# Optimization experiments

Hardware: AMD Instinct MI355X
Metric: run time of the kernel (lower is better)

## Reference

```python
import jax, jax.numpy as jnp
import numpy as np

NF = 64      # num_feat
NFR = 5      # num_frames
G = 8        # offset/deformable groups
CENTER = NFR // 2
K = 9        # 3x3 taps


def conv3x3(x, w, b):
    y = jax.lax.conv_general_dilated(x, w, (1, 1), 'SAME',
                                     dimension_numbers=('NCHW', 'OIHW', 'NCHW'))
    return y + b[None, :, None, None]


def mdcn(x, offsets, masks, w, b):
    # x: [B,C,H,W]; offsets: [B,2*G*K,H,W] (layout g,k,(y,x)); masks: [B,G*K,H,W]
    B, C, H, W = x.shape
    Cg = C // G
    off = offsets.reshape(B, G, K, 2, H, W)
    oy, ox = off[:, :, :, 0], off[:, :, :, 1]          # [B,G,K,H,W]
    m = masks.reshape(B, G, K, H, W)
    ky = jnp.repeat(jnp.arange(3), 3) - 1              # [K]
    kx = jnp.tile(jnp.arange(3), 3) - 1
    base_y = (ky[:, None, None] + jnp.arange(H)[None, :, None]).astype(x.dtype)  # [K,H,1]
    base_x = (kx[:, None, None] + jnp.arange(W)[None, None, :]).astype(x.dtype)  # [K,1,W]
    py = oy + base_y[None, None]                        # [B,G,K,H,W]
    px = ox + base_x[None, None]
    y0f = jnp.floor(py); x0f = jnp.floor(px)
    ty = py - y0f; tx = px - x0f
    y0 = y0f.astype(jnp.int32); x0 = x0f.astype(jnp.int32)
    xg = x.reshape(B, G, Cg, H * W)

    def gather(yi, xi):
        valid = (yi >= 0) & (yi < H) & (xi >= 0) & (xi < W)
        yc = jnp.clip(yi, 0, H - 1); xc = jnp.clip(xi, 0, W - 1)
        idx = (yc * W + xc).reshape(B, G, 1, K * H * W)
        idx = jnp.broadcast_to(idx, (B, G, Cg, K * H * W))
        v = jnp.take_along_axis(xg, idx, axis=3).reshape(B, G, Cg, K, H, W)
        return v * valid.reshape(B, G, 1, K, H, W)

    v00 = gather(y0, x0); v01 = gather(y0, x0 + 1)
    v10 = gather(y0 + 1, x0); v11 = gather(y0 + 1, x0 + 1)
    ty_ = ty[:, :, None]; tx_ = tx[:, :, None]          # [B,G,1,K,H,W]
    samp = (v00 * (1 - ty_) * (1 - tx_) + v01 * (1 - ty_) * tx_ +
            v10 * ty_ * (1 - tx_) + v11 * ty_ * tx_)
    samp = samp * m[:, :, None]                          # modulation
    wr = w.reshape(-1, G, Cg, K)                         # [Cout,G,Cg,K]
    out = jnp.einsum('bgckhw,ogck->bohw', samp, wr)
    return out + b[None, :, None, None]


def setup_inputs():
    key = jax.random.key(0)
    ks = jax.random.split(key, 16)
    def mk(k, shape, fan_in):
        return jax.random.normal(k, shape, jnp.float32) * (1.0 / np.sqrt(fan_in))
    B, H, W = 1, 160, 160
    return {
        'x':   jax.random.normal(ks[0], (B, NFR, 4, H, W), jnp.float32),
        'fw1': mk(ks[1], (NF, 4, 3, 3), 4 * 9),   'fb1': jnp.zeros((NF,), jnp.float32),
        'fw2': mk(ks[2], (NF, NF, 3, 3), NF * 9), 'fb2': jnp.zeros((NF,), jnp.float32),
        'fw3': mk(ks[3], (NF, NF, 3, 3), NF * 9), 'fb3': jnp.zeros((NF,), jnp.float32),
        'ow1': mk(ks[4], (NF, 2 * NF, 3, 3), 2 * NF * 9), 'ob1': jnp.zeros((NF,), jnp.float32),
        'ow2': mk(ks[5], (NF, NF, 3, 3), NF * 9),         'ob2': jnp.zeros((NF,), jnp.float32),
        'ow3': mk(ks[6], (G * 27, NF, 3, 3), NF * 9) * 0.1,
        'ob3': jnp.zeros((G * 27,), jnp.float32),
        'dw':  mk(ks[7], (NF, NF, 3, 3), NF * 9), 'db': jnp.zeros((NF,), jnp.float32),
    }


def reference(x, fw1, fb1, fw2, fb2, fw3, fb3, ow1, ob1, ow2, ob2, ow3, ob3, dw, db):
    B, N, C, H, W = x.shape
    f = x.reshape(B * N, C, H, W)
    f = jax.nn.relu(conv3x3(f, fw1, fb1))
    f = jax.nn.relu(conv3x3(f, fw2, fb2))
    f = jax.nn.relu(conv3x3(f, fw3, fb3))
    feats = f.reshape(B, N, NF, H, W)
    ref = feats[:, CENTER]                               # [B,NF,H,W]
    nc = np.array([i for i in range(N) if i != CENTER])
    curr = feats[:, nc].reshape(B * (N - 1), NF, H, W)
    ref_t = jnp.broadcast_to(ref[:, None], (B, N - 1, NF, H, W)).reshape(B * (N - 1), NF, H, W)
    cat = jnp.concatenate([ref_t, curr], axis=1)         # [B(N-1),2*NF,H,W]
    o = jax.nn.relu(conv3x3(cat, ow1, ob1))
    o = jax.nn.relu(conv3x3(o, ow2, ob2))
    raw = conv3x3(o, ow3, ob3)                           # [B(N-1),27G,H,W]
    offsets = raw[:, :G * 18]
    masks = jax.nn.sigmoid(raw[:, G * 18:])
    aligned = mdcn(curr, offsets, masks, dw, db)
    aligned = aligned.reshape(B, N - 1, NF, H, W)
    return jnp.concatenate([aligned[:, :CENTER], ref[:, None], aligned[:, CENTER:]], axis=1)
```

## Files before the change

### kernel.cpp

```cpp
#include <hip/hip_runtime.h>
#include <hip/hip_bf16.h>
#include <math.h>

#define HH 160
#define WW 160
#define HWsz (HH*WW)

typedef short bf16x8 __attribute__((ext_vector_type(8)));
typedef float f32x4  __attribute__((ext_vector_type(4)));

__device__ inline ushort f2bf(float f) {
    unsigned int u = __float_as_uint(f);
    unsigned int r = (u + 0x7FFFu + ((u >> 16) & 1u)) >> 16;
    return (ushort)r;
}

__device__ inline void unpk8(uint4 u, float* f) {
    f[0] = __uint_as_float(u.x << 16); f[1] = __uint_as_float(u.x & 0xFFFF0000u);
    f[2] = __uint_as_float(u.y << 16); f[3] = __uint_as_float(u.y & 0xFFFF0000u);
    f[4] = __uint_as_float(u.z << 16); f[5] = __uint_as_float(u.z & 0xFFFF0000u);
    f[6] = __uint_as_float(u.w << 16); f[7] = __uint_as_float(u.w & 0xFFFF0000u);
}

__global__ __launch_bounds__(256)
void pack_all(const float* __restrict__ fw2, const float* __restrict__ fw3,
              const float* __restrict__ ow1, const float* __restrict__ ow2,
              const float* __restrict__ ow3,
              ushort* __restrict__ w2p, ushort* __restrict__ w3p,
              ushort* __restrict__ o1p, ushort* __restrict__ o2p,
              ushort* __restrict__ o3p)
{
    const int seg = blockIdx.y;
    const float* w; ushort* wp; int Cout, Cin, MT_TOT, CIC;
    switch (seg) {
        case 0: w = fw2; wp = w2p; Cout = 64;  Cin = 64;  MT_TOT = 4;  CIC = 2; break;
        case 1: w = fw3; wp = w3p; Cout = 64;  Cin = 64;  MT_TOT = 4;  CIC = 2; break;
        case 2: w = ow1; wp = o1p; Cout = 64;  Cin = 128; MT_TOT = 4;  CIC = 4; break;
        case 3: w = ow2; wp = o2p; Cout = 64;  Cin = 64;  MT_TOT = 4;  CIC = 2; break;
        default: w = ow3; wp = o3p; Cout = 216; Cin = 64; MT_TOT = 16; CIC = 2; break;
    }
    const int idx = blockIdx.x * 256 + threadIdx.x;
    const int total = 9 * CIC * MT_TOT * 64;
    if (idx >= total) return;
    const int lane = idx & 63;
    int t = idx >> 6;
    const int mt  = t % MT_TOT; t /= MT_TOT;
    const int cic = t % CIC;    t /= CIC;
    const int tap = t;
    const int co  = mt * 16 + (lane & 15);
    const int ci0 = cic * 32 + (lane >> 4) * 8;
    ushort v[8];
#pragma unroll
    for (int j = 0; j < 8; ++j) {
        const int ci = ci0 + j;
        float f = 0.f;
        if (co < Cout && ci < Cin) f = w[((size_t)co * Cin + ci) * 9 + tap];
        v[j] = f2bf(f);
    }
    uint4 pk;
    pk.x = (unsigned)v[0] | ((unsigned)v[1] << 16);
    pk.y = (unsigned)v[2] | ((unsigned)v[3] << 16);
    pk.z = (unsigned)v[4] | ((unsigned)v[5] << 16);
    pk.w = (unsigned)v[6] | ((unsigned)v[7] << 16);
    *(uint4*)(wp + (size_t)idx * 8) = pk;
}

__global__ __launch_bounds__(256)
void pack_dw_mfma(const float* __restrict__ dw, ushort* __restrict__ wmp)
{
    const int idx = blockIdx.x * 256 + threadIdx.x;
    if (idx >= 18 * 4 * 64) return;
    const int lane = idx & 63;
    const int mt   = (idx >> 6) & 3;
    const int chunk = idx >> 8;
    const int o  = mt * 16 + (lane & 15);
    const int gk = chunk * 4 + (lane >> 4);
    const int g  = gk / 9, k = gk % 9;
    ushort v[8];
#pragma unroll
    for (int j = 0; j < 8; ++j)
        v[j] = f2bf(dw[((size_t)o * 64 + g * 8 + j) * 9 + k]);
    uint4 pk;
    pk.x = (unsigned)v[0] | ((unsigned)v[1] << 16);
    pk.y = (unsigned)v[2] | ((unsigned)v[3] << 16);
    pk.z = (unsigned)v[4] | ((unsigned)v[5] << 16);
    pk.w = (unsigned)v[6] | ((unsigned)v[7] << 16);
    *(uint4*)(wmp + (size_t)idx * 8) = pk;
}

template<int CIC_TILE, int CI_STEPS, bool CONCAT, bool RELU, int OMODE>
__global__ __launch_bounds__(256, 3)
void mfma_conv(const ushort* __restrict__ in, const ushort* __restrict__ wp,
               const float* __restrict__ bias, void* __restrict__ outv,
               int Cout, int MT_TOT, int COG)
{
    constexpr int ROWS = 8, HR = ROWS + 2, NT = 4;
    constexpr int C8   = CIC_TILE * 4;
    constexpr int CICT = CIC_TILE * CI_STEPS;
    constexpr int CIN  = CICT * 32;
    __shared__ uint4 s_in4[HR * 34 * C8];

    const int tid = threadIdx.x;
    const int lane = tid & 63, wid = tid >> 6;
    const int lane15 = lane & 15, lgrp = lane >> 4;
    const int bz = blockIdx.z;
    const int frame = bz / COG, cog = bz % COG;
    const int x0 = blockIdx.x * 32, y0 = blockIdx.y * ROWS;

    const ushort* src = nullptr; const ushort* srcRef = nullptr; const ushort* srcCur = nullptr;
    if (CONCAT) {
        const int fidx = (frame < 2) ? frame : frame + 1;
        srcRef = in + (size_t)2 * HWsz * 64;
        srcCur = in + (size_t)fidx * HWsz * 64;
    } else {
        src = in + (size_t)frame * HWsz * CIN;
    }

    f32x4 acc[4][NT];
#pragma unroll
    for (int m = 0; m < 4; ++m)
#pragma unroll
        for (int n = 0; n < NT; ++n) acc[m][n] = (f32x4){0.f, 0.f, 0.f, 0.f};

    const uint4* wp4 = (const uint4*)wp;
    const int wrow = wid * 2;
    const int mtg0 = cog * 4;

    for (int step = 0; step < CI_STEPS; ++step) {
        if (step) __syncthreads();
        for (int i = tid; i < HR * 34 * C8; i += 256) {
            const int ci8l = i & (C8 - 1);
            const int rem = i / C8;
            const int col = rem % 34, row = rem / 34;
            const int gy = y0 + row - 1, gx = x0 + col - 1;
            const int gci8 = step * C8 + ci8l;
            uint4 v = {0u, 0u, 0u, 0u};
            if (gy >= 0 && gy < HH && gx >= 0 && gx < WW) {
                if (CONCAT) {
                    const ushort* sp = (gci8 < 8) ? srcRef : srcCur;
                    v = *(const uint4*)(sp + (size_t)(gy * WW + gx) * 64 + (gci8 & 7) * 8);
                } else {
                    v = *(const uint4*)(src + (size_t)(gy * WW + gx) * CIN + gci8 * 8);
                }
            }
            s_in4[(row * 34 + col) * C8 + (ci8l ^ (col & 7))] = v;
        }
        __syncthreads();

#pragma unroll 3
        for (int tap = 0; tap < 9; ++tap) {
            const int dy  = tap / 3 - 1;
            const int dxp = tap % 3;
#pragma unroll
            for (int cic = 0; cic < CIC_TILE; ++cic) {
                const uint4* ap = wp4 +
                    ((size_t)(tap * CICT + step * CIC_TILE + cic) * MT_TOT + mtg0) * 64 + lane;
                bf16x8 a[4];
#pragma unroll
                for (int mt = 0; mt < 4; ++mt)
                    a[mt] = *(const bf16x8*)(ap + (size_t)mt * 64);
#pragma unroll
                for (int nt = 0; nt < NT; ++nt) {
                    const int row_l = wrow + (nt >> 1) + dy + 1;
                    const int col_l = (nt & 1) * 16 + lane15 + dxp;
                    const bf16x8 b = *(const bf16x8*)
                        &s_in4[(row_l * 34 + col_l) * C8 + ((cic * 4 + lgrp) ^ (col_l & 7))];
#pragma unroll
                    for (int mt = 0; mt < 4; ++mt)
                        acc[mt][nt] = __builtin_amdgcn_mfma_f32_16x16x32_bf16(a[mt], b, acc[mt][nt], 0, 0, 0);
                }
            }
        }
    }

#pragma unroll
    for (int mt = 0; mt < 4; ++mt) {
        const int co = cog * 64 + mt * 16 + lgrp * 4;
        if (co < Cout) {
            const float4 bs = *(const float4*)&bias[co];
#pragma unroll
            for (int nt = 0; nt < NT; ++nt) {
                const int yy = y0 + wrow + (nt >> 1);
                const int xx = x0 + (nt & 1) * 16 + lane15;
                f32x4 v = acc[mt][nt];
                v[0] += bs.x; v[1] += bs.y; v[2] += bs.z; v[3] += bs.w;
                if (RELU) {
                    v[0] = fmaxf(v[0], 0.f); v[1] = fmaxf(v[1], 0.f);
                    v[2] = fmaxf(v[2], 0.f); v[3] = fmaxf(v[3], 0.f);
                }
                if (OMODE == 0) {
                    const size_t po = ((size_t)frame * HWsz + yy * WW + xx) * (size_t)Cout + co;
                    uint2 pk;
                    pk.x = (unsigned)f2bf(v[0]) | ((unsigned)f2bf(v[1]) << 16);
                    pk.y = (unsigned)f2bf(v[2]) | ((unsigned)f2bf(v[3]) << 16);
                    *(uint2*)((ushort*)outv + po) = pk;
                } else {
                    float* of = (float*)outv;
                    const size_t base = ((size_t)frame * Cout + co) * HWsz + yy * WW + xx;
#pragma unroll
                    for (int j = 0; j < 4; ++j)
                        of[base + (size_t)j * HWsz] = v[j];
                }
            }
        }
    }
}

__global__ __launch_bounds__(256)
void conv1_kernel(const float* __restrict__ x, const float* __restrict__ w,
                  const float* __restrict__ b, ushort* __restrict__ out)
{
    const int fr = blockIdx.z;
    const int t = threadIdx.x;
    const int tx = t & 15, ty = t >> 4;
    const int x0 = blockIdx.x * 16, y0 = blockIdx.y * 16;

    __shared__ float s_x[4][18][18];
    __shared__ float s_w[36][64];
    __shared__ float s_b[64];

    for (int i = t; i < 4 * 18 * 18; i += 256) {
        const int ci = i / 324, rem = i % 324;
        const int yy = rem / 18, xx = rem % 18;
        const int gy = y0 + yy - 1, gx = x0 + xx - 1;
        float v = 0.f;
        if (gy >= 0 && gy < HH && gx >= 0 && gx < WW)
            v = x[((size_t)fr * 4 + ci) * HWsz + gy * WW + gx];
        s_x[ci][yy][xx] = v;
    }
    for (int i = t; i < 36 * 64; i += 256) {
        const int row = i / 64, o = i % 64;
        const int ci = row / 9, tap = row % 9;
        s_w[row][o] = w[((size_t)o * 4 + ci) * 9 + tap];
    }
    if (t < 64) s_b[t] = b[t];
    __syncthreads();

    float acc[64];
#pragma unroll
    for (int i = 0; i < 64; ++i) acc[i] = 0.f;

#pragma unroll
    for (int ci = 0; ci < 4; ++ci) {
#pragma unroll
        for (int tap = 0; tap < 9; ++tap) {
            const float v = s_x[ci][ty + tap / 3][tx + tap % 3];
            const float4* wr = (const float4*)&s_w[ci * 9 + tap][0];
#pragma unroll
            for (int o4 = 0; o4 < 16; ++o4) {
                const float4 wv = wr[o4];
                acc[o4 * 4 + 0] = fmaf(v, wv.x, acc[o4 * 4 + 0]);
                acc[o4 * 4 + 1] = fmaf(v, wv.y, acc[o4 * 4 + 1]);
                acc[o4 * 4 + 2] = fmaf(v, wv.z, acc[o4 * 4 + 2]);
                acc[o4 * 4 + 3] = fmaf(v, wv.w, acc[o4 * 4 + 3]);
            }
        }
    }

    ushort* ob = out + ((size_t)fr * HWsz + (y0 + ty) * WW + (x0 + tx)) * 64;
#pragma unroll
    for (int o8 = 0; o8 < 8; ++o8) {
        ushort v[8];
#pragma unroll
        for (int j = 0; j < 8; ++j)
            v[j] = f2bf(fmaxf(acc[o8 * 8 + j] + s_b[o8 * 8 + j], 0.f));
        uint4 pk;
        pk.x = (unsigned)v[0] | ((unsigned)v[1] << 16);
        pk.y = (unsigned)v[2] | ((unsigned)v[3] << 16);
        pk.z = (unsigned)v[4] | ((unsigned)v[5] << 16);
        pk.w = (unsigned)v[6] | ((unsigned)v[7] << 16);
        *(uint4*)(ob + o8 * 8) = pk;
    }
}

__global__ __launch_bounds__(256)
void copy_ref_kernel(const ushort* __restrict__ fts, float* __restrict__ out)
{
    const int px = blockIdx.x * 256 + threadIdx.x;
    if (px >= HWsz) return;
    const uint4* p = (const uint4*)(fts + ((size_t)2 * HWsz + px) * 64);
    float* ob = out + (size_t)2 * 64 * HWsz + px;
#pragma unroll
    for (int o8 = 0; o8 < 8; ++o8) {
        float f[8];
        unpk8(p[o8], f);
#pragma unroll
        for (int j = 0; j < 8; ++j)
            ob[(size_t)(o8 * 8 + j) * HWsz] = f[j];
    }
}

__global__ __launch_bounds__(256)
void repack_feats(const ushort* __restrict__ fts, ushort* __restrict__ ftsg)
{
    const int px = blockIdx.x * 256 + threadIdx.x;
    const int b  = blockIdx.y;
    if (px >= HWsz) return;
    const int fidx = (b < 2) ? b : b + 1;
    const uint4* src = (const uint4*)(fts + ((size_t)fidx * HWsz + px) * 64);
    uint4 v[8];
#pragma unroll
    for (int g = 0; g < 8; ++g) v[g] = src[g];
#pragma unroll
    for (int g = 0; g < 8; ++g)
        *(uint4*)(ftsg + ((size_t)(b * 8 + g) * HWsz + px) * 8) = v[g];
}

__global__ __launch_bounds__(256)
void mdcn_mfma(const ushort* __restrict__ ftsg, const float* __restrict__ rawc,
               const ushort* __restrict__ wmp, const float* __restrict__ db,
               float* __restrict__ out)
{
    const int b    = blockIdx.z;
    const int fidx = (b < 2) ? b : b + 1;
    const int tid  = threadIdx.x;
    const int lane = tid & 63, wid = tid >> 6;
    const int lane15 = lane & 15, lgrp = lane >> 4;
    const int x = blockIdx.x * 16 + lane15;
    const int y = blockIdx.y * 4 + wid;
    const int hw = y * WW + x;

    const float* rawb = rawc + (size_t)b * 216 * HWsz;
    const uint4* wmp4 = (const uint4*)wmp;

    f32x4 acc[4];
#pragma unroll
    for (int m = 0; m < 4; ++m) acc[m] = (f32x4){0.f, 0.f, 0.f, 0.f};

    for (int chunk = 0; chunk < 18; ++chunk) {
        const int gk = chunk * 4 + lgrp;
        const int g  = gk / 9, k = gk - 9 * g;
        const int kyy = k / 3 - 1, kxx = k % 3 - 1;

        const float oy = rawb[(size_t)(g * 18 + 2 * k + 0) * HWsz + hw];
        const float ox = rawb[(size_t)(g * 18 + 2 * k + 1) * HWsz + hw];
        float mv = rawb[(size_t)(144 + g * 9 + k) * HWsz + hw];
        mv = 1.f / (1.f + __expf(-mv));

        const float py = oy + (float)(y + kyy);
        const float px = ox + (float)(x + kxx);
        const float y0f = floorf(py), x0f = floorf(px);
        const float tyf = py - y0f, txf = px - x0f;
        const int y0 = (int)y0f, x0i = (int)x0f;
        const int y1 = y0 + 1, x1 = x0i + 1;
        const bool vy0 = (y0 >= 0) & (y0 < HH);
        const bool vy1 = (y1 >= 0) & (y1 < HH);
        const bool vx0 = (x0i >= 0) & (x0i < WW);
        const bool vx1 = (x1 >= 0) & (x1 < WW);
        const int yc0 = min(max(y0, 0), HH - 1), yc1 = min(max(y1, 0), HH - 1);
        const int xc0 = min(max(x0i, 0), WW - 1), xc1 = min(max(x1, 0), WW - 1);
        float w00 = (1.f - tyf) * (1.f - txf) * mv;
        float w01 = (1.f - tyf) * txf * mv;
        float w10 = tyf * (1.f - txf) * mv;
        float w11 = tyf * txf * mv;
        if (!(vy0 && vx0)) w00 = 0.f;
        if (!(vy0 && vx1)) w01 = 0.f;
        if (!(vy1 && vx0)) w10 = 0.f;
        if (!(vy1 && vx1)) w11 = 0.f;

        const ushort* pb = ftsg + (size_t)(b * 8 + g) * HWsz * 8;
        const uint4 u00 = *(const uint4*)(pb + (size_t)(yc0 * WW + xc0) * 8);
        const uint4 u01 = *(const uint4*)(pb + (size_t)(yc0 * WW + xc1) * 8);
        const uint4 u10 = *(const uint4*)(pb + (size_t)(yc1 * WW + xc0) * 8);
        const uint4 u11 = *(const uint4*)(pb + (size_t)(yc1 * WW + xc1) * 8);
        float f00[8], f01[8], f10[8], f11[8];
        unpk8(u00, f00); unpk8(u01, f01); unpk8(u10, f10); unpk8(u11, f11);

        bf16x8 bfrag;
#pragma unroll
        for (int c = 0; c < 8; ++c) {
            const float v = fmaf(w11, f11[c], fmaf(w10, f10[c],
                             fmaf(w01, f01[c], w00 * f00[c])));
            bfrag[c] = (short)f2bf(v);
        }

#pragma unroll
        for (int mt = 0; mt < 4; ++mt) {
            const bf16x8 a = *(const bf16x8*)&wmp4[(size_t)(chunk * 4 + mt) * 64 + lane];
            acc[mt] = __builtin_amdgcn_mfma_f32_16x16x32_bf16(a, bfrag, acc[mt], 0, 0, 0);
        }
    }

    float* ob = out + (size_t)fidx * 64 * HWsz + hw;
#pragma unroll
    for (int mt = 0; mt < 4; ++mt) {
        const int o0 = mt * 16 + lgrp * 4;
        const float4 bs = *(const float4*)&db[o0];
        ob[(size_t)(o0 + 0) * HWsz] = acc[mt][0] + bs.x;
        ob[(size_t)(o0 + 1) * HWsz] = acc[mt][1] + bs.y;
        ob[(size_t)(o0 + 2) * HWsz] = acc[mt][2] + bs.z;
        ob[(size_t)(o0 + 3) * HWsz] = acc[mt][3] + bs.w;
    }
}

extern "C" void kernel_launch(void* const* d_in, const int* in_sizes, int n_in,
                              void* d_out, int out_size, void* d_ws, size_t ws_size,
                              hipStream_t stream)
{
    const float* x   = (const float*)d_in[0];
    const float* fw1 = (const float*)d_in[1];
    const float* fb1 = (const float*)d_in[2];
    const float* fw2 = (const float*)d_in[3];
    const float* fb2 = (const float*)d_in[4];
    const float* fw3 = (const float*)d_in[5];
    const float* fb3 = (const float*)d_in[6];
    const float* ow1 = (const float*)d_in[7];
    const float* ob1 = (const float*)d_in[8];
    const float* ow2 = (const float*)d_in[9];
    const float* ob2 = (const float*)d_in[10];
    const float* ow3 = (const float*)d_in[11];
    const float* ob3 = (const float*)d_in[12];
    const float* dw  = (const float*)d_in[13];
    const float* db  = (const float*)d_in[14];
    float* out = (float*)d_out;

    ushort* buf1 = (ushort*)d_ws;
    ushort* buf2 = buf1 + (size_t)5 * HWsz * 64;
    ushort* fts  = buf2 + (size_t)5 * HWsz * 64;
    ushort* ftsg = fts + (size_t)5 * HWsz * 64;
    float*  raw  = (float*)(ftsg + (size_t)4 * 8 * HWsz * 8);
    ushort* w2p  = (ushort*)(raw + (size_t)4 * HWsz * 216);
    ushort* w3p  = w2p + 36864;
    ushort* o1p  = w3p + 36864;
    ushort* o2p  = o1p + 73728;
    ushort* o3p  = o2p + 36864;
    ushort* wmp  = o3p + 147456;

    const dim3 blk(256);

    pack_all<<<dim3(72, 5), blk, 0, stream>>>(fw2, fw3, ow1, ow2, ow3,
                                              w2p, w3p, o1p, o2p, o3p);
    pack_dw_mfma<<<dim3(18), blk, 0, stream>>>(dw, wmp);

    conv1_kernel<<<dim3(10, 10, 5), blk, 0, stream>>>(x, fw1, fb1, buf1);
    mfma_conv<2, 1, false, true, 0><<<dim3(5, 20, 5), blk, 0, stream>>>(
        buf1, w2p, fb2, buf2, 64, 4, 1);
    mfma_conv<2, 1, false, true, 0><<<dim3(5, 20, 5), blk, 0, stream>>>(
        buf2, w3p, fb3, fts, 64, 4, 1);

    copy_ref_kernel<<<dim3(100), blk, 0, stream>>>(fts, out);
    repack_feats<<<dim3(100, 4), blk, 0, stream>>>(fts, ftsg);

    mfma_conv<2, 2, true, true, 0><<<dim3(5, 20, 4), blk, 0, stream>>>(
        fts, o1p, ob1, buf1, 64, 4, 1);
    mfma_conv<2, 1, false, true, 0><<<dim3(5, 20, 4), blk, 0, stream>>>(
        buf1, o2p, ob2, buf2, 64, 4, 1);
    mfma_conv<2, 1, false, false, 2><<<dim3(5, 20, 16), blk, 0, stream>>>(
        buf2, o3p, ob3, raw, 216, 16, 4);

    mdcn_mfma<<<dim3(10, 40, 4), blk, 0, stream>>>(ftsg, raw, wmp, db, out);
}
```

Before: 226.0 us.

## Fuse ref-copy and group repack into conv epilogue; pack offsets as bf16

The last feature conv epilogue now writes the center frame directly to the fp32 output and the neighbour frames into the group-major layout, which removes the copy_ref and repack_feats kernels. The offset/mask conv now writes bf16 values interleaved as (oy,ox,mask) per group-tap, so mdcn reads them with one 8-byte load instead of three strided fp32 loads. The dw pack kernel is folded into pack_all to save a launch, and mdcn uses hardware packed bf16 conversion and unroll 2. Storing offsets in bf16 loses precision in the sampling positions and could hurt accuracy.

```diff
diff --git a/kernel.cpp b/kernel.cpp
--- a/kernel.cpp
+++ b/kernel.cpp
@@ -25,12 +25,35 @@
 __global__ __launch_bounds__(256)
 void pack_all(const float* __restrict__ fw2, const float* __restrict__ fw3,
               const float* __restrict__ ow1, const float* __restrict__ ow2,
-              const float* __restrict__ ow3,
+              const float* __restrict__ ow3, const float* __restrict__ dw,
               ushort* __restrict__ w2p, ushort* __restrict__ w3p,
               ushort* __restrict__ o1p, ushort* __restrict__ o2p,
-              ushort* __restrict__ o3p)
+              ushort* __restrict__ o3p, ushort* __restrict__ wmp)
 {
     const int seg = blockIdx.y;
+    const int idx = blockIdx.x * 256 + threadIdx.x;
+
+    if (seg == 5) {
+        if (idx >= 18 * 4 * 64) return;
+        const int lane = idx & 63;
+        const int mt   = (idx >> 6) & 3;
+        const int chunk = idx >> 8;
+        const int o  = mt * 16 + (lane & 15);
+        const int gk = chunk * 4 + (lane >> 4);
+        const int g  = gk / 9, k = gk % 9;
+        ushort v[8];
+#pragma unroll
+        for (int j = 0; j < 8; ++j)
+            v[j] = f2bf(dw[((size_t)o * 64 + g * 8 + j) * 9 + k]);
+        uint4 pk;
+        pk.x = (unsigned)v[0] | ((unsigned)v[1] << 16);
+        pk.y = (unsigned)v[2] | ((unsigned)v[3] << 16);
+        pk.z = (unsigned)v[4] | ((unsigned)v[5] << 16);
+        pk.w = (unsigned)v[6] | ((unsigned)v[7] << 16);
+        *(uint4*)(wmp + (size_t)idx * 8) = pk;
+        return;
+    }
+
     const float* w; ushort* wp; int Cout, Cin, MT_TOT, CIC;
     switch (seg) {
         case 0: w = fw2; wp = w2p; Cout = 64;  Cin = 64;  MT_TOT = 4;  CIC = 2; break;
@@ -39,7 +62,6 @@
         case 3: w = ow2; wp = o2p; Cout = 64;  Cin = 64;  MT_TOT = 4;  CIC = 2; break;
         default: w = ow3; wp = o3p; Cout = 216; Cin = 64; MT_TOT = 16; CIC = 2; break;
     }
-    const int idx = blockIdx.x * 256 + threadIdx.x;
     const int total = 9 * CIC * MT_TOT * 64;
     if (idx >= total) return;
     const int lane = idx & 63;
@@ -65,34 +87,12 @@
     *(uint4*)(wp + (size_t)idx * 8) = pk;
 }
 
-__global__ __launch_bounds__(256)
-void pack_dw_mfma(const float* __restrict__ dw, ushort* __restrict__ wmp)
-{
-    const int idx = blockIdx.x * 256 + threadIdx.x;
-    if (idx >= 18 * 4 * 64) return;
-    const int lane = idx & 63;
-    const int mt   = (idx >> 6) & 3;
-    const int chunk = idx >> 8;
-    const int o  = mt * 16 + (lane & 15);
-    const int gk = chunk * 4 + (lane >> 4);
-    const int g  = gk / 9, k = gk % 9;
-    ushort v[8];
-#pragma unroll
-    for (int j = 0; j < 8; ++j)
-        v[j] = f2bf(dw[((size_t)o * 64 + g * 8 + j) * 9 + k]);
-    uint4 pk;
-    pk.x = (unsigned)v[0] | ((unsigned)v[1] << 16);
-    pk.y = (unsigned)v[2] | ((unsigned)v[3] << 16);
-    pk.z = (unsigned)v[4] | ((unsigned)v[5] << 16);
-    pk.w = (unsigned)v[6] | ((unsigned)v[7] << 16);
-    *(uint4*)(wmp + (size_t)idx * 8) = pk;
-}
-
 template<int CIC_TILE, int CI_STEPS, bool CONCAT, bool RELU, int OMODE>
 __global__ __launch_bounds__(256, 3)
 void mfma_conv(const ushort* __restrict__ in, const ushort* __restrict__ wp,
                const float* __restrict__ bias, void* __restrict__ outv,
-               int Cout, int MT_TOT, int COG)
+               int Cout, int MT_TOT, int COG,
+               float* __restrict__ outmain, ushort* __restrict__ ftsg)
 {
     constexpr int ROWS = 8, HR = ROWS + 2, NT = 4;
     constexpr int C8   = CIC_TILE * 4;
@@ -182,24 +182,44 @@
             for (int nt = 0; nt < NT; ++nt) {
                 const int yy = y0 + wrow + (nt >> 1);
                 const int xx = x0 + (nt & 1) * 16 + lane15;
+                const int hw = yy * WW + xx;
                 f32x4 v = acc[mt][nt];
                 v[0] += bs.x; v[1] += bs.y; v[2] += bs.z; v[3] += bs.w;
                 if (RELU) {
                     v[0] = fmaxf(v[0], 0.f); v[1] = fmaxf(v[1], 0.f);
                     v[2] = fmaxf(v[2], 0.f); v[3] = fmaxf(v[3], 0.f);
                 }
-                if (OMODE == 0) {
-                    const size_t po = ((size_t)frame * HWsz + yy * WW + xx) * (size_t)Cout + co;
+                if (OMODE <= 1) {
                     uint2 pk;
                     pk.x = (unsigned)f2bf(v[0]) | ((unsigned)f2bf(v[1]) << 16);
                     pk.y = (unsigned)f2bf(v[2]) | ((unsigned)f2bf(v[3]) << 16);
-                    *(uint2*)((ushort*)outv + po) = pk;
+                    *(uint2*)((ushort*)outv + ((size_t)frame * HWsz + hw) * 64 + co) = pk;
+                    if (OMODE == 1) {
+                        if (frame == 2) {
+#pragma unroll
+                            for (int j = 0; j < 4; ++j)
+                                outmain[((size_t)(128 + co + j)) * HWsz + hw] = v[j];
+                        } else {
+                            const int b = (frame < 2) ? frame : frame - 1;
+                            *(uint2*)(ftsg + (((size_t)(b * 8 + (co >> 3)) * HWsz + hw) * 8 + (co & 7))) = pk;
+                        }
+                    }
                 } else {
-                    float* of = (float*)outv;
-                    const size_t base = ((size_t)frame * Cout + co) * HWsz + yy * WW + xx;
-#pragma unroll
-                    for (int j = 0; j < 4; ++j)
-                        of[base + (size_t)j * HWsz] = v[j];
+                    ushort* rawp = (ushort*)outv + (size_t)frame * 72 * HWsz * 4;
+                    const ushort h0 = f2bf(v[0]), h1 = f2bf(v[1]);
+                    const ushort h2 = f2bf(v[2]), h3 = f2bf(v[3]);
+                    if (co < 144) {
+                        *(unsigned*)(rawp + ((size_t)(co >> 1) * HWsz + hw) * 4) =
+                            (unsigned)h0 | ((unsigned)h1 << 16);
+                        *(unsigned*)(rawp + ((size_t)((co >> 1) + 1) * HWsz + hw) * 4) =
+                            (unsigned)h2 | ((unsigned)h3 << 16);
+                    } else {
+                        const int gk0 = co - 144;
+                        rawp[((size_t)(gk0 + 0) * HWsz + hw) * 4 + 2] = h0;
+                        rawp[((size_t)(gk0 + 1) * HWsz + hw) * 4 + 2] = h1;
+                        rawp[((size_t)(gk0 + 2) * HWsz + hw) * 4 + 2] = h2;
+                        rawp[((size_t)(gk0 + 3) * HWsz + hw) * 4 + 2] = h3;
+                    }
                 }
             }
         }
@@ -274,40 +294,7 @@
 }
 
 __global__ __launch_bounds__(256)
-void copy_ref_kernel(const ushort* __restrict__ fts, float* __restrict__ out)
-{
-    const int px = blockIdx.x * 256 + threadIdx.x;
-    if (px >= HWsz) return;
-    const uint4* p = (const uint4*)(fts + ((size_t)2 * HWsz + px) * 64);
-    float* ob = out + (size_t)2 * 64 * HWsz + px;
-#pragma unroll
-    for (int o8 = 0; o8 < 8; ++o8) {
-        float f[8];
-        unpk8(p[o8], f);
-#pragma unroll
-        for (int j = 0; j < 8; ++j)
-            ob[(size_t)(o8 * 8 + j) * HWsz] = f[j];
-    }
-}
-
-__global__ __launch_bounds__(256)
-void repack_feats(const ushort* __restrict__ fts, ushort* __restrict__ ftsg)
-{
-    const int px = blockIdx.x * 256 + threadIdx.x;
-    const int b  = blockIdx.y;
-    if (px >= HWsz) return;
-    const int fidx = (b < 2) ? b : b + 1;
-    const uint4* src = (const uint4*)(fts + ((size_t)fidx * HWsz + px) * 64);
-    uint4 v[8];
-#pragma unroll
-    for (int g = 0; g < 8; ++g) v[g] = src[g];
-#pragma unroll
-    for (int g = 0; g < 8; ++g)
-        *(uint4*)(ftsg + ((size_t)(b * 8 + g) * HWsz + px) * 8) = v[g];
-}
-
-__global__ __launch_bounds__(256)
-void mdcn_mfma(const ushort* __restrict__ ftsg, const float* __restrict__ rawc,
+void mdcn_mfma(const ushort* __restrict__ ftsg, const ushort* __restrict__ rawpk,
                const ushort* __restrict__ wmp, const float* __restrict__ db,
                float* __restrict__ out)
 {
@@ -320,22 +307,24 @@
     const int y = blockIdx.y * 4 + wid;
     const int hw = y * WW + x;
 
-    const float* rawb = rawc + (size_t)b * 216 * HWsz;
+    const ushort* rawb = rawpk + (size_t)b * 72 * HWsz * 4;
     const uint4* wmp4 = (const uint4*)wmp;
 
     f32x4 acc[4];
 #pragma unroll
     for (int m = 0; m < 4; ++m) acc[m] = (f32x4){0.f, 0.f, 0.f, 0.f};
 
+#pragma unroll 2
     for (int chunk = 0; chunk < 18; ++chunk) {
         const int gk = chunk * 4 + lgrp;
         const int g  = gk / 9, k = gk - 9 * g;
         const int kyy = k / 3 - 1, kxx = k % 3 - 1;
 
-        const float oy = rawb[(size_t)(g * 18 + 2 * k + 0) * HWsz + hw];
-        const float ox = rawb[(size_t)(g * 18 + 2 * k + 1) * HWsz + hw];
-        float mv = rawb[(size_t)(144 + g * 9 + k) * HWsz + hw];
-        mv = 1.f / (1.f + __expf(-mv));
+        const uint2 rr = *(const uint2*)(rawb + ((size_t)gk * HWsz + hw) * 4);
+        const float oy = __uint_as_float(rr.x << 16);
+        const float ox = __uint_as_float(rr.x & 0xFFFF0000u);
+        const float mraw = __uint_as_float(rr.y << 16);
+        const float mv = 1.f / (1.f + __expf(-mraw));
 
         const float py = oy + (float)(y + kyy);
         const float px = ox + (float)(x + kxx);
@@ -349,10 +338,11 @@
         const bool vx1 = (x1 >= 0) & (x1 < WW);
         const int yc0 = min(max(y0, 0), HH - 1), yc1 = min(max(y1, 0), HH - 1);
         const int xc0 = min(max(x0i, 0), WW - 1), xc1 = min(max(x1, 0), WW - 1);
-        float w00 = (1.f - tyf) * (1.f - txf) * mv;
-        float w01 = (1.f - tyf) * txf * mv;
-        float w10 = tyf * (1.f - txf) * mv;
-        float w11 = tyf * txf * mv;
+        const float a0 = (1.f - tyf) * mv, a1 = tyf * mv;
+        float w00 = a0 * (1.f - txf);
+        float w01 = a0 * txf;
+        float w10 = a1 * (1.f - txf);
+        float w11 = a1 * txf;
         if (!(vy0 && vx0)) w00 = 0.f;
         if (!(vy0 && vx1)) w01 = 0.f;
         if (!(vy1 && vx0)) w10 = 0.f;
@@ -366,13 +356,17 @@
         float f00[8], f01[8], f10[8], f11[8];
         unpk8(u00, f00); unpk8(u01, f01); unpk8(u10, f10); unpk8(u11, f11);
 
-        bf16x8 bfrag;
-#pragma unroll
-        for (int c = 0; c < 8; ++c) {
-            const float v = fmaf(w11, f11[c], fmaf(w10, f10[c],
-                             fmaf(w01, f01[c], w00 * f00[c])));
-            bfrag[c] = (short)f2bf(v);
-        }
+        float s[8];
+#pragma unroll
+        for (int c = 0; c < 8; ++c)
+            s[c] = fmaf(w11, f11[c], fmaf(w10, f10[c],
+                    fmaf(w01, f01[c], w00 * f00[c])));
+        uint4 bpk;
+        asm("v_cvt_pk_bf16_f32 %0, %1, %2" : "=v"(bpk.x) : "v"(s[0]), "v"(s[1]));
+        asm("v_cvt_pk_bf16_f32 %0, %1, %2" : "=v"(bpk.y) : "v"(s[2]), "v"(s[3]));
+        asm("v_cvt_pk_bf16_f32 %0, %1, %2" : "=v"(bpk.z) : "v"(s[4]), "v"(s[5]));
+        asm("v_cvt_pk_bf16_f32 %0, %1, %2" : "=v"(bpk.w) : "v"(s[6]), "v"(s[7]));
+        const bf16x8 bfrag = __builtin_bit_cast(bf16x8, bpk);
 
 #pragma unroll
         for (int mt = 0; mt < 4; ++mt) {
@@ -418,8 +412,8 @@
     ushort* buf2 = buf1 + (size_t)5 * HWsz * 64;
     ushort* fts  = buf2 + (size_t)5 * HWsz * 64;
     ushort* ftsg = fts + (size_t)5 * HWsz * 64;
-    float*  raw  = (float*)(ftsg + (size_t)4 * 8 * HWsz * 8);
-    ushort* w2p  = (ushort*)(raw + (size_t)4 * HWsz * 216);
+    ushort* raw  = ftsg + (size_t)4 * 8 * HWsz * 8;
+    ushort* w2p  = raw + (size_t)4 * 72 * HWsz * 4;
     ushort* w3p  = w2p + 36864;
     ushort* o1p  = w3p + 36864;
     ushort* o2p  = o1p + 73728;
@@ -428,25 +422,21 @@
 
     const dim3 blk(256);
 
-    pack_all<<<dim3(72, 5), blk, 0, stream>>>(fw2, fw3, ow1, ow2, ow3,
-                                              w2p, w3p, o1p, o2p, o3p);
-    pack_dw_mfma<<<dim3(18), blk, 0, stream>>>(dw, wmp);
+    pack_all<<<dim3(72, 6), blk, 0, stream>>>(fw2, fw3, ow1, ow2, ow3, dw,
+                                              w2p, w3p, o1p, o2p, o3p, wmp);
 
     conv1_kernel<<<dim3(10, 10, 5), blk, 0, stream>>>(x, fw1, fb1, buf1);
     mfma_conv<2, 1, false, true, 0><<<dim3(5, 20, 5), blk, 0, stream>>>(
-        buf1, w2p, fb2, buf2, 64, 4, 1);
-    mfma_conv<2, 1, false, true, 0><<<dim3(5, 20, 5), blk, 0, stream>>>(
-        buf2, w3p, fb3, fts, 64, 4, 1);
-
-    copy_ref_kernel<<<dim3(100), blk, 0, stream>>>(fts, out);
-    repack_feats<<<dim3(100, 4), blk, 0, stream>>>(fts, ftsg);
+        buf1, w2p, fb2, buf2, 64, 4, 1, nullptr, nullptr);
+    mfma_conv<2, 1, false, true, 1><<<dim3(5, 20, 5), blk, 0, stream>>>(
+        buf2, w3p, fb3, fts, 64, 4, 1, out, ftsg);
 
     mfma_conv<2, 2, true, true, 0><<<dim3(5, 20, 4), blk, 0, stream>>>(
-        fts, o1p, ob1, buf1, 64, 4, 1);
+        fts, o1p, ob1, buf1, 64, 4, 1, nullptr, nullptr);
     mfma_conv<2, 1, false, true, 0><<<dim3(5, 20, 4), blk, 0, stream>>>(
-        buf1, o2p, ob2, buf2, 64, 4, 1);
-    mfma_conv<2, 1, false, false, 2><<<dim3(5, 20, 16), blk, 0, stream>>>(
-        buf2, o3p, ob3, raw, 216, 16, 4);
+        buf1, o2p, ob2, buf2, 64, 4, 1, nullptr, nullptr);
+    mfma_conv<2, 1, false, false, 3><<<dim3(5, 20, 16), blk, 0, stream>>>(
+        buf2, o3p, ob3, raw, 216, 16, 4, nullptr, nullptr);
 
     mdcn_mfma<<<dim3(10, 40, 4), blk, 0, stream>>>(ftsg, raw, wmp, db, out);
 }
```

New measurement: 216.6 us. 4.2% less time.
